# Kernel tuning notes

Hardware: AMD Instinct MI355X
Metric: run time of the kernel (lower is better)

Reference implementation:

```python
import jax, jax.numpy as jnp
import numpy as np
from jax import lax


def setup_inputs() -> dict:
    key = jax.random.key(0)
    k1, k2 = jax.random.split(key)
    N, dim, m = 8192, 1024, 1024
    x = jax.random.normal(k1, (N, dim), dtype=jnp.float32)
    vectors = jax.random.normal(k2, (m, dim), dtype=jnp.float32) * 0.01
    bias = jnp.zeros((dim,), dtype=jnp.float32)
    return {"x": x, "vectors": vectors, "bias": bias}


def reference(x, vectors, bias):
    # Normalize each reflection vector to unit length: [m, d]
    v_normed = vectors / jnp.linalg.norm(vectors, axis=1, keepdims=True)

    def step(out, v):
        # out: [N, d], v: [d]
        proj = out @ v                       # [N]
        out = out - 2.0 * proj[:, None] * v  # rank-1 Householder update
        return out, None

    out, _ = lax.scan(step, x, v_normed)
    return out + bias
```

## Files before the change

### kernel.cpp

```cpp
#include <hip/hip_runtime.h>
#include <hip/hip_bf16.h>

typedef __attribute__((ext_vector_type(8))) short short8;
typedef __attribute__((ext_vector_type(4))) short s16x4;
typedef __attribute__((ext_vector_type(4))) float f32x4;

static __device__ inline short f2bf(float f) {
    unsigned u = __float_as_uint(f);
    unsigned r = (u + 0x7fffu + ((u >> 16) & 1u)) >> 16;
    return (short)r;
}
static __device__ inline float bf2f(short h) {
    return __uint_as_float(((unsigned)(unsigned short)h) << 16);
}

static __device__ inline int swz32(int row, int slot) {
    return row * 32 + ((slot ^ ((row >> 1) & 3)) << 3);
}
static __device__ inline int swz64(int row, int slot) {
    return row * 64 + ((slot ^ (row & 7)) << 3);
}

__global__ __launch_bounds__(256) void k_prepall(const float* __restrict__ vec,
                                                 short* __restrict__ Vh,
                                                 short* __restrict__ Vth,
                                                 int m, int dim) {
    __shared__ float tile[8][1028];
    __shared__ float ps[8][32];
    __shared__ float invs[8];
    int r0 = blockIdx.x * 8;
    int t = threadIdx.x;
    int rt = t >> 5, ct = t & 31;
    float ss = 0.f;
#pragma unroll
    for (int p = 0; p < 8; ++p) {
        int c = p * 128 + ct * 4;
        float4 v = *(const float4*)&vec[(size_t)(r0 + rt) * dim + c];
        *(float4*)&tile[rt][c] = v;
        ss += v.x * v.x + v.y * v.y + v.z * v.z + v.w * v.w;
    }
    ps[rt][ct] = ss;
    __syncthreads();
    if (t < 8) {
        float s = 0.f;
#pragma unroll
        for (int q = 0; q < 32; ++q) s += ps[t][q];
        invs[t] = 1.0f / sqrtf(s);
    }
    __syncthreads();
    float iv = invs[rt];
#pragma unroll
    for (int p = 0; p < 8; ++p) {
        int c = p * 128 + ct * 4;
        s16x4 h;
#pragma unroll
        for (int q = 0; q < 4; ++q) h[q] = f2bf(tile[rt][c + q] * iv);
        *(s16x4*)&Vh[(size_t)(r0 + rt) * dim + c] = h;
    }
#pragma unroll
    for (int cc = 0; cc < 4; ++cc) {
        int c = t * 4 + cc;
        s16x4 h0, h1;
#pragma unroll
        for (int r = 0; r < 4; ++r) h0[r] = f2bf(tile[r][c] * invs[r]);
#pragma unroll
        for (int r = 0; r < 4; ++r) h1[r] = f2bf(tile[4 + r][c] * invs[4 + r]);
        *(s16x4*)&Vth[(size_t)c * m + r0] = h0;
        *(s16x4*)&Vth[(size_t)c * m + r0 + 4] = h1;
    }
}

template<int MODE, int TRI, int CH>
__global__ __launch_bounds__(256) void k_nt64pc(
    const short* __restrict__ Ah, const short* __restrict__ Al,
    const short* __restrict__ Bh, const short* __restrict__ Bl,
    float* __restrict__ Cf, short* __restrict__ Ch, short* __restrict__ Cl,
    int K, int lda, int ldb, int ldc, int gw, int nTiles,
    const float* __restrict__ castX, short* __restrict__ castXh, int castN4) {
    __shared__ short As[2][2][64 * 32];
    __shared__ short Bs[2][2][64 * 32];
    int flat = blockIdx.x;
    if (flat >= nTiles) {
        int idx = (flat - nTiles) * 256 + threadIdx.x;
        int stride = (gridDim.x - nTiles) * 256;
        for (int i = idx; i < castN4; i += stride) {
            float4 v = ((const float4*)castX)[i];
            float f[4] = {v.x, v.y, v.z, v.w};
            s16x4 h;
#pragma unroll
            for (int q = 0; q < 4; ++q) h[q] = f2bf(f[q]);
            *(s16x4*)&castXh[(size_t)i * 4] = h;
        }
        return;
    }
    int i0 = (flat / gw) * 64, j0 = (flat % gw) * 64;
    if (TRI == 2 && j0 < i0) return;
    int KE = (TRI == 1) ? (j0 + 64) : K;
    int t = threadIdx.x, lane = t & 63, wave = t >> 6;
    int wr = wave >> 1, wc = wave & 1;
    int srow = t >> 2, slot = t & 3;
    int sofs = swz32(srow, slot);
    int gofs = slot * 8;
    const short* gA_h = &Ah[(size_t)(i0 + srow) * lda + gofs];
    const short* gA_l = (CH >= 3) ? &Al[(size_t)(i0 + srow) * lda + gofs] : nullptr;
    const short* gB_h = &Bh[(size_t)(j0 + srow) * ldb + gofs];
    const short* gB_l = (CH >= 2) ? &Bl[(size_t)(j0 + srow) * ldb + gofs] : nullptr;
    short8 pAh = *(const short8*)&gA_h[0];
    short8 pAl, pBl;
    short8 pBh = *(const short8*)&gB_h[0];
    if (CH >= 2) pBl = *(const short8*)&gB_l[0];
    if (CH >= 3) pAl = *(const short8*)&gA_l[0];
    *(short8*)&As[0][0][sofs] = pAh;
    *(short8*)&Bs[0][0][sofs] = pBh;
    if (CH >= 2) *(short8*)&Bs[0][1][sofs] = pBl;
    if (CH >= 3) *(short8*)&As[0][1][sofs] = pAl;
    f32x4 acc[2][2] = {};
    int nIter = KE >> 5;
    int cur = 0;
    for (int it = 0; it < nIter; ++it) {
        __syncthreads();
        int kn = (it + 1) << 5;
        bool have = kn < KE;
        if (have) {
            pAh = *(const short8*)&gA_h[kn];
            pBh = *(const short8*)&gB_h[kn];
            if (CH >= 2) pBl = *(const short8*)&gB_l[kn];
            if (CH >= 3) pAl = *(const short8*)&gA_l[kn];
        }
        int g = lane >> 4;
        short8 ah[2], al2[2], bh[2], bl2[2];
#pragma unroll
        for (int i = 0; i < 2; ++i) {
            int ro = swz32(wr * 32 + i * 16 + (lane & 15), g);
            ah[i] = *(const short8*)&As[cur][0][ro];
            if (CH >= 3) al2[i] = *(const short8*)&As[cur][1][ro];
        }
#pragma unroll
        for (int j = 0; j < 2; ++j) {
            int ro = swz32(wc * 32 + j * 16 + (lane & 15), g);
            bh[j] = *(const short8*)&Bs[cur][0][ro];
            if (CH >= 2) bl2[j] = *(const short8*)&Bs[cur][1][ro];
        }
#pragma unroll
        for (int i = 0; i < 2; ++i)
#pragma unroll
            for (int j = 0; j < 2; ++j) {
                acc[i][j] = __builtin_amdgcn_mfma_f32_16x16x32_bf16(ah[i], bh[j], acc[i][j], 0, 0, 0);
                if (CH >= 2)
                    acc[i][j] = __builtin_amdgcn_mfma_f32_16x16x32_bf16(ah[i], bl2[j], acc[i][j], 0, 0, 0);
                if (CH >= 3)
                    acc[i][j] = __builtin_amdgcn_mfma_f32_16x16x32_bf16(al2[i], bh[j], acc[i][j], 0, 0, 0);
            }
        if (have) {
            *(short8*)&As[cur ^ 1][0][sofs] = pAh;
            *(short8*)&Bs[cur ^ 1][0][sofs] = pBh;
            if (CH >= 2) *(short8*)&Bs[cur ^ 1][1][sofs] = pBl;
            if (CH >= 3) *(short8*)&As[cur ^ 1][1][sofs] = pAl;
        }
        cur ^= 1;
    }
#pragma unroll
    for (int i = 0; i < 2; ++i)
#pragma unroll
        for (int j = 0; j < 2; ++j) {
            int row0 = i0 + wr * 32 + i * 16 + ((lane >> 4) << 2);
            int col = j0 + wc * 32 + j * 16 + (lane & 15);
#pragma unroll
            for (int r = 0; r < 4; ++r) {
                float v = acc[i][j][r];
                size_t idx = (size_t)(row0 + r) * ldc + col;
                if (MODE == 2) {
                    Ch[idx] = f2bf((((row0 + r) == col) ? 1.f : 0.f) - v);
                } else if (MODE == 1) {
                    Ch[idx] = f2bf(v);
                } else {
                    short h = f2bf(v);
                    Ch[idx] = h;
                    Cl[idx] = f2bf(v - bf2f(h));
                    Cf[idx] = v;
                }
            }
        }
}

__global__ __launch_bounds__(256) void k_baseinv2(const float* __restrict__ G,
                                                  short* __restrict__ Th, short* __restrict__ Tl,
                                                  short* __restrict__ Tth, short* __restrict__ Ttl,
                                                  int m) {
    __shared__ float Rs[64 * 64];
    int d = blockIdx.x >> 4, g = blockIdx.x & 15;
    int b0 = d * 64;
    int t = threadIdx.x, lane = t & 63, wave = t >> 6;
    {
        int r = t >> 2, c00 = (t & 3) * 16;
#pragma unroll
        for (int q = 0; q < 4; ++q)
            *(float4*)&Rs[r * 64 + c00 + q * 4] =
                *(const float4*)&G[(size_t)(b0 + r) * m + b0 + c00 + q * 4];
    }
    __syncthreads();
    int c = g * 4 + wave;
    float x = 0.f;
    for (int r = c; r >= 0; --r) {
        float prod = Rs[r * 64 + lane] * x;
        float s = prod;
#pragma unroll
        for (int off = 32; off; off >>= 1) s += __shfl_xor(s, off, 64);
        if (lane == r) x = ((r == c) ? 2.f : 0.f) - 2.f * s;
    }
    short h = f2bf(x);
    short l = f2bf(x - bf2f(h));
    Th[(size_t)(b0 + lane) * m + b0 + c] = h;
    Tl[(size_t)(b0 + lane) * m + b0 + c] = l;
    Tth[(size_t)(b0 + c) * m + b0 + lane] = h;
    Ttl[(size_t)(b0 + c) * m + b0 + lane] = l;
}

__global__ __launch_bounds__(256) void k_tree64f(const float* __restrict__ G,
                                                 short* __restrict__ Th, short* __restrict__ Tl,
                                                 short* __restrict__ Tth, short* __restrict__ Ttl,
                                                 int m) {
    __shared__ float Gb[64 * 65];
    __shared__ float Ai[64 * 65];
    __shared__ float Ci[64 * 64];
    __shared__ float Tm[64 * 64];
    int p = blockIdx.x;
    int a0 = p * 128, c0 = a0 + 64;
    int t = threadIdx.x;
    {
        int r = t >> 2, c00 = (t & 3) * 16;
#pragma unroll
        for (int q = 0; q < 4; ++q) {
            *(float4*)&Gb[r * 65 + c00 + q * 4] =
                *(const float4*)&G[(size_t)(a0 + r) * m + c0 + c00 + q * 4];
            s16x4 ha = *(const s16x4*)&Th[(size_t)(a0 + r) * m + a0 + c00 + q * 4];
            s16x4 la = *(const s16x4*)&Tl[(size_t)(a0 + r) * m + a0 + c00 + q * 4];
            s16x4 hc = *(const s16x4*)&Th[(size_t)(c0 + r) * m + c0 + c00 + q * 4];
            s16x4 lc = *(const s16x4*)&Tl[(size_t)(c0 + r) * m + c0 + c00 + q * 4];
#pragma unroll
            for (int e = 0; e < 4; ++e) {
                Ai[r * 65 + c00 + q * 4 + e] = bf2f(ha[e]) + bf2f(la[e]);
                Ci[r * 64 + c00 + q * 4 + e] = bf2f(hc[e]) + bf2f(lc[e]);
            }
        }
    }
    __syncthreads();
    int tx = t & 15, ty = t >> 4;
    float acc[4][4] = {};
#pragma unroll 4
    for (int k = 0; k < 64; ++k) {
        float av[4], bv[4];
#pragma unroll
        for (int i = 0; i < 4; ++i) av[i] = Gb[(ty * 4 + i) * 65 + k];
#pragma unroll
        for (int j = 0; j < 4; ++j) bv[j] = Ci[k * 64 + tx * 4 + j];
#pragma unroll
        for (int i = 0; i < 4; ++i)
#pragma unroll
            for (int j = 0; j < 4; ++j) acc[i][j] += av[i] * bv[j];
    }
#pragma unroll
    for (int i = 0; i < 4; ++i)
#pragma unroll
        for (int j = 0; j < 4; ++j) Tm[(ty * 4 + i) * 64 + tx * 4 + j] = acc[i][j];
    __syncthreads();
    float acc2[4][4] = {};
#pragma unroll 4
    for (int k = 0; k < 64; ++k) {
        float av[4], bv[4];
#pragma unroll
        for (int i = 0; i < 4; ++i) av[i] = Ai[(ty * 4 + i) * 65 + k];
#pragma unroll
        for (int j = 0; j < 4; ++j) bv[j] = Tm[k * 64 + tx * 4 + j];
#pragma unroll
        for (int i = 0; i < 4; ++i)
#pragma unroll
            for (int j = 0; j < 4; ++j) acc2[i][j] += av[i] * bv[j];
    }
#pragma unroll
    for (int i = 0; i < 4; ++i)
#pragma unroll
        for (int j = 0; j < 4; ++j) {
            float v = -acc2[i][j];
            short h = f2bf(v);
            short l = f2bf(v - bf2f(h));
            int R = a0 + ty * 4 + i, C = c0 + tx * 4 + j;
            Th[(size_t)R * m + C] = h;
            Tl[(size_t)R * m + C] = l;
            Tth[(size_t)C * m + R] = h;
            Ttl[(size_t)C * m + R] = l;
        }
}

template<int PHASE>
__global__ __launch_bounds__(256) void k_trimm(
    const short* __restrict__ Ah, const short* __restrict__ Al,
    const short* __restrict__ Bh, const short* __restrict__ Bl,
    short* __restrict__ C1h, short* __restrict__ C1l,
    short* __restrict__ C2h, short* __restrict__ C2l,
    int m, int s) {
    __shared__ short As[2][64 * 32];
    __shared__ short Bs[2][64 * 32];
    int p = blockIdx.z;
    int a0 = 2 * p * s, c0 = a0 + s;
    int r0 = blockIdx.y * 64, ct = blockIdx.x * 64;
    int KS = (PHASE == 1) ? 0 : r0;
    int KE = (PHASE == 1) ? (ct + 64) : s;
    size_t tbase = (size_t)p * s * s;
    int t = threadIdx.x, lane = t & 63, wave = t >> 6;
    int wr = wave >> 1, wc = wave & 1;
    int srow = t >> 2, slot = t & 3;
    int sofs = swz32(srow, slot);
    int gofs = slot * 8;
    f32x4 acc[2][2] = {};
    for (int k0 = KS; k0 < KE; k0 += 32) {
        __syncthreads();
        if (PHASE == 1) {
            *(short8*)&As[0][sofs] = *(const short8*)&Ah[(size_t)(a0 + r0 + srow) * m + c0 + k0 + gofs];
            *(short8*)&As[1][sofs] = *(const short8*)&Al[(size_t)(a0 + r0 + srow) * m + c0 + k0 + gofs];
            *(short8*)&Bs[0][sofs] = *(const short8*)&Bh[(size_t)(c0 + ct + srow) * m + c0 + k0 + gofs];
            *(short8*)&Bs[1][sofs] = *(const short8*)&Bl[(size_t)(c0 + ct + srow) * m + c0 + k0 + gofs];
        } else {
            *(short8*)&As[0][sofs] = *(const short8*)&Ah[(size_t)(a0 + r0 + srow) * m + a0 + k0 + gofs];
            *(short8*)&As[1][sofs] = *(const short8*)&Al[(size_t)(a0 + r0 + srow) * m + a0 + k0 + gofs];
            *(short8*)&Bs[0][sofs] = *(const short8*)&Bh[tbase + (size_t)(ct + srow) * s + k0 + gofs];
            *(short8*)&Bs[1][sofs] = *(const short8*)&Bl[tbase + (size_t)(ct + srow) * s + k0 + gofs];
        }
        __syncthreads();
        int g = lane >> 4;
        short8 ah[2], al2[2], bh[2], bl2[2];
#pragma unroll
        for (int i = 0; i < 2; ++i) {
            int ro = swz32(wr * 32 + i * 16 + (lane & 15), g);
            ah[i] = *(const short8*)&As[0][ro];
            al2[i] = *(const short8*)&As[1][ro];
        }
#pragma unroll
        for (int j = 0; j < 2; ++j) {
            int ro = swz32(wc * 32 + j * 16 + (lane & 15), g);
            bh[j] = *(const short8*)&Bs[0][ro];
            bl2[j] = *(const short8*)&Bs[1][ro];
        }
#pragma unroll
        for (int i = 0; i < 2; ++i)
#pragma unroll
            for (int j = 0; j < 2; ++j) {
                acc[i][j] = __builtin_amdgcn_mfma_f32_16x16x32_bf16(ah[i], bh[j], acc[i][j], 0, 0, 0);
                acc[i][j] = __builtin_amdgcn_mfma_f32_16x16x32_bf16(ah[i], bl2[j], acc[i][j], 0, 0, 0);
                acc[i][j] = __builtin_amdgcn_mfma_f32_16x16x32_bf16(al2[i], bh[j], acc[i][j], 0, 0, 0);
            }
    }
#pragma unroll
    for (int i = 0; i < 2; ++i)
#pragma unroll
        for (int j = 0; j < 2; ++j) {
            int row0 = r0 + wr * 32 + i * 16 + ((lane >> 4) << 2);
            int col = ct + wc * 32 + j * 16 + (lane & 15);
#pragma unroll
            for (int r = 0; r < 4; ++r) {
                if (PHASE == 1) {
                    float v = acc[i][j][r];
                    short h = f2bf(v);
                    short l = f2bf(v - bf2f(h));
                    size_t idx = tbase + (size_t)col * s + row0 + r;
                    C1h[idx] = h;
                    C1l[idx] = l;
                } else {
                    float v = -acc[i][j][r];
                    short h = f2bf(v);
                    short l = f2bf(v - bf2f(h));
                    int R = a0 + row0 + r, Cc = c0 + col;
                    C1h[(size_t)R * m + Cc] = h;
                    C1l[(size_t)R * m + Cc] = l;
                    C2h[(size_t)Cc * m + R] = h;
                    C2l[(size_t)Cc * m + R] = l;
                }
            }
        }
}

__global__ __launch_bounds__(256) void k_apply3(const short* __restrict__ xh,
                                                const short* __restrict__ Qt,
                                                const float* __restrict__ bias,
                                                float* __restrict__ out, int dim) {
    __shared__ short As[128 * 64];
    __shared__ short Bs[128 * 64];
    int nwg = gridDim.x * gridDim.y;
    int flat = blockIdx.y * gridDim.x + blockIdx.x;
    int cpx = nwg >> 3;
    int L = (flat & 7) * cpx + (flat >> 3);
    int m0 = (L / gridDim.x) * 128, n0 = (L % gridDim.x) * 128;
    int t = threadIdx.x, lane = t & 63, wave = t >> 6;
    int wr = wave >> 1, wc = wave & 1;
    int sr = lane >> 3;
    int sslot = (lane & 7) ^ (sr & 7);
    f32x4 acc[4][4] = {};
    for (int k0 = 0; k0 < dim; k0 += 64) {
        __syncthreads();
#pragma unroll
        for (int q = 0; q < 4; ++q) {
            int rg = wave * 4 + q;
            int row = rg * 8 + sr;
            const short* gA = &xh[(size_t)(m0 + row) * dim + k0 + sslot * 8];
            const short* gB = &Qt[(size_t)(n0 + row) * dim + k0 + sslot * 8];
            __builtin_amdgcn_global_load_lds(
                (const __attribute__((address_space(1))) void*)gA,
                (__attribute__((address_space(3))) void*)&As[rg * 8 * 64], 16, 0, 0);
            __builtin_amdgcn_global_load_lds(
                (const __attribute__((address_space(1))) void*)gB,
                (__attribute__((address_space(3))) void*)&Bs[rg * 8 * 64], 16, 0, 0);
        }
        __syncthreads();
#pragma unroll
        for (int kk = 0; kk < 2; ++kk) {
            int g = kk * 4 + (lane >> 4);
            short8 af[4], bf_[4];
#pragma unroll
            for (int i = 0; i < 4; ++i)
                af[i] = *(const short8*)&As[swz64(wr * 64 + i * 16 + (lane & 15), g)];
#pragma unroll
            for (int j = 0; j < 4; ++j)
                bf_[j] = *(const short8*)&Bs[swz64(wc * 64 + j * 16 + (lane & 15), g)];
#pragma unroll
            for (int i = 0; i < 4; ++i)
#pragma unroll
                for (int j = 0; j < 4; ++j)
                    acc[i][j] = __builtin_amdgcn_mfma_f32_16x16x32_bf16(af[i], bf_[j], acc[i][j], 0, 0, 0);
        }
    }
#pragma unroll
    for (int i = 0; i < 4; ++i)
#pragma unroll
        for (int j = 0; j < 4; ++j) {
            int row = m0 + wr * 64 + i * 16 + (lane >> 4) * 4;
            int col = n0 + wc * 64 + j * 16 + (lane & 15);
            float b = bias[col];
#pragma unroll
            for (int r = 0; r < 4; ++r)
                out[(size_t)(row + r) * dim + col] = acc[i][j][r] + b;
        }
}

extern "C" void kernel_launch(void* const* d_in, const int* in_sizes, int n_in,
                              void* d_out, int out_size, void* d_ws, size_t ws_size,
                              hipStream_t stream) {
    const float* x = (const float*)d_in[0];
    const float* vec = (const float*)d_in[1];
    const float* bias = (const float*)d_in[2];
    float* out = (float*)d_out;

    int dim = in_sizes[2];
    int m = in_sizes[1] / dim;
    int n = in_sizes[0] / dim;

    const size_t MD = (size_t)m * dim;
    const size_t MM = (size_t)m * m;

    char* cur = (char*)d_ws;
    auto alloc_f = [&](size_t nelem) { float* p = (float*)cur; cur += nelem * 4; return p; };
    auto alloc_s = [&](size_t nelem) { short* p = (short*)cur; cur += nelem * 2; return p; };
    float* G   = alloc_f(MM);
    short* Vh  = alloc_s(MD);
    short* Vth = alloc_s(MD);
    short* Gh  = alloc_s(MM);
    short* Gl  = alloc_s(MM);
    short* Th  = alloc_s(MM);
    short* Tl  = alloc_s(MM);
    short* Tth = alloc_s(MM);
    short* Ttl = alloc_s(MM);
    short* Wh  = alloc_s(MD);
    short* Qt  = alloc_s((size_t)dim * dim);
    short* tmph = alloc_s(MM / 2);
    short* tmpl = alloc_s(MM / 2);
    short* xh  = alloc_s((size_t)n * dim);

    int gw = m / 64;
    int nTiles = gw * gw;
    int castN4 = (int)((size_t)n * dim / 4);

    k_prepall<<<m / 8, 256, 0, stream>>>(vec, Vh, Vth, m, dim);

    k_nt64pc<3, 2, 1><<<nTiles + 512, 256, 0, stream>>>(Vh, nullptr, Vh, nullptr, G, Gh, Gl,
                                                        dim, dim, dim, m, gw, nTiles,
                                                        x, xh, castN4);
    k_baseinv2<<<(m / 64) * 16, 256, 0, stream>>>(G, Th, Tl, Tth, Ttl, m);
    k_tree64f<<<m / 128, 256, 0, stream>>>(G, Th, Tl, Tth, Ttl, m);
    for (int s = 128; s < m; s <<= 1) {
        dim3 g(s / 64, s / 64, m / (2 * s));
        k_trimm<1><<<g, 256, 0, stream>>>(Gh, Gl, Tth, Ttl, tmph, tmpl, nullptr, nullptr, m, s);
        k_trimm<2><<<g, 256, 0, stream>>>(Th, Tl, tmph, tmpl, Th, Tl, Tth, Ttl, m, s);
    }

    k_nt64pc<1, 1, 2><<<(m / 64) * (dim / 64), 256, 0, stream>>>(Vth, nullptr, Tth, Ttl, nullptr, Wh, nullptr,
                                                                 m, m, m, m, m / 64, (m / 64) * (dim / 64),
                                                                 nullptr, nullptr, 0);
    k_nt64pc<2, 0, 1><<<(dim / 64) * (dim / 64), 256, 0, stream>>>(Vth, nullptr, Wh, nullptr, nullptr, Qt, nullptr,
                                                                   m, m, m, dim, dim / 64, (dim / 64) * (dim / 64),
                                                                   nullptr, nullptr, 0);

    k_apply3<<<dim3(dim / 128, n / 128), 256, 0, stream>>>(xh, Qt, bias, out, dim);
}
```

Baseline: 150.1 us.

## Fuse triangular-inverse tree stages into one persistent kernel with grid barriers

Replaces the base-inverse kernel, the 64-block tree kernel and the sequence of per-level trimm launches with a single persistent kernel. Its 256 blocks synchronize through an atomic-counter global barrier, and the counter is zeroed inside the preceding Gram kernel. This removes about 16 kernel launch gaps on a chain of small, latency-bound stages. In exchange it depends on all 256 blocks being co-resident, and the spin barrier has a timeout guard that could silently break correctness if residency fails.

```diff
diff --git a/kernel.cpp b/kernel.cpp
--- a/kernel.cpp
+++ b/kernel.cpp
@@ -19,6 +19,21 @@
 }
 static __device__ inline int swz64(int row, int slot) {
     return row * 64 + ((slot ^ (row & 7)) << 3);
+}
+
+static __device__ inline void gbar(unsigned* cnt, unsigned target) {
+    __syncthreads();
+    if (threadIdx.x == 0) {
+        __threadfence();
+        __hip_atomic_fetch_add(cnt, 1u, __ATOMIC_ACQ_REL, __HIP_MEMORY_SCOPE_AGENT);
+        long guard = 0;
+        while (__hip_atomic_load(cnt, __ATOMIC_ACQUIRE, __HIP_MEMORY_SCOPE_AGENT) < target) {
+            __builtin_amdgcn_s_sleep(2);
+            if (++guard > (1L << 25)) break;
+        }
+        __threadfence();
+    }
+    __syncthreads();
 }
 
 __global__ __launch_bounds__(256) void k_prepall(const float* __restrict__ vec,
@@ -76,11 +91,13 @@
     const short* __restrict__ Bh, const short* __restrict__ Bl,
     float* __restrict__ Cf, short* __restrict__ Ch, short* __restrict__ Cl,
     int K, int lda, int ldb, int ldc, int gw, int nTiles,
-    const float* __restrict__ castX, short* __restrict__ castXh, int castN4) {
+    const float* __restrict__ castX, short* __restrict__ castXh, int castN4,
+    unsigned* zeroCnt) {
     __shared__ short As[2][2][64 * 32];
     __shared__ short Bs[2][2][64 * 32];
     int flat = blockIdx.x;
     if (flat >= nTiles) {
+        if (zeroCnt && flat == nTiles && threadIdx.x == 0) *zeroCnt = 0u;
         int idx = (flat - nTiles) * 256 + threadIdx.x;
         int stride = (gridDim.x - nTiles) * 256;
         for (int i = idx; i < castN4; i += stride) {
@@ -183,127 +200,16 @@
         }
 }
 
-__global__ __launch_bounds__(256) void k_baseinv2(const float* __restrict__ G,
-                                                  short* __restrict__ Th, short* __restrict__ Tl,
-                                                  short* __restrict__ Tth, short* __restrict__ Ttl,
-                                                  int m) {
-    __shared__ float Rs[64 * 64];
-    int d = blockIdx.x >> 4, g = blockIdx.x & 15;
-    int b0 = d * 64;
-    int t = threadIdx.x, lane = t & 63, wave = t >> 6;
-    {
-        int r = t >> 2, c00 = (t & 3) * 16;
-#pragma unroll
-        for (int q = 0; q < 4; ++q)
-            *(float4*)&Rs[r * 64 + c00 + q * 4] =
-                *(const float4*)&G[(size_t)(b0 + r) * m + b0 + c00 + q * 4];
-    }
-    __syncthreads();
-    int c = g * 4 + wave;
-    float x = 0.f;
-    for (int r = c; r >= 0; --r) {
-        float prod = Rs[r * 64 + lane] * x;
-        float s = prod;
-#pragma unroll
-        for (int off = 32; off; off >>= 1) s += __shfl_xor(s, off, 64);
-        if (lane == r) x = ((r == c) ? 2.f : 0.f) - 2.f * s;
-    }
-    short h = f2bf(x);
-    short l = f2bf(x - bf2f(h));
-    Th[(size_t)(b0 + lane) * m + b0 + c] = h;
-    Tl[(size_t)(b0 + lane) * m + b0 + c] = l;
-    Tth[(size_t)(b0 + c) * m + b0 + lane] = h;
-    Ttl[(size_t)(b0 + c) * m + b0 + lane] = l;
-}
-
-__global__ __launch_bounds__(256) void k_tree64f(const float* __restrict__ G,
-                                                 short* __restrict__ Th, short* __restrict__ Tl,
-                                                 short* __restrict__ Tth, short* __restrict__ Ttl,
-                                                 int m) {
-    __shared__ float Gb[64 * 65];
-    __shared__ float Ai[64 * 65];
-    __shared__ float Ci[64 * 64];
-    __shared__ float Tm[64 * 64];
-    int p = blockIdx.x;
-    int a0 = p * 128, c0 = a0 + 64;
-    int t = threadIdx.x;
-    {
-        int r = t >> 2, c00 = (t & 3) * 16;
-#pragma unroll
-        for (int q = 0; q < 4; ++q) {
-            *(float4*)&Gb[r * 65 + c00 + q * 4] =
-                *(const float4*)&G[(size_t)(a0 + r) * m + c0 + c00 + q * 4];
-            s16x4 ha = *(const s16x4*)&Th[(size_t)(a0 + r) * m + a0 + c00 + q * 4];
-            s16x4 la = *(const s16x4*)&Tl[(size_t)(a0 + r) * m + a0 + c00 + q * 4];
-            s16x4 hc = *(const s16x4*)&Th[(size_t)(c0 + r) * m + c0 + c00 + q * 4];
-            s16x4 lc = *(const s16x4*)&Tl[(size_t)(c0 + r) * m + c0 + c00 + q * 4];
-#pragma unroll
-            for (int e = 0; e < 4; ++e) {
-                Ai[r * 65 + c00 + q * 4 + e] = bf2f(ha[e]) + bf2f(la[e]);
-                Ci[r * 64 + c00 + q * 4 + e] = bf2f(hc[e]) + bf2f(lc[e]);
-            }
-        }
-    }
-    __syncthreads();
-    int tx = t & 15, ty = t >> 4;
-    float acc[4][4] = {};
-#pragma unroll 4
-    for (int k = 0; k < 64; ++k) {
-        float av[4], bv[4];
-#pragma unroll
-        for (int i = 0; i < 4; ++i) av[i] = Gb[(ty * 4 + i) * 65 + k];
-#pragma unroll
-        for (int j = 0; j < 4; ++j) bv[j] = Ci[k * 64 + tx * 4 + j];
-#pragma unroll
-        for (int i = 0; i < 4; ++i)
-#pragma unroll
-            for (int j = 0; j < 4; ++j) acc[i][j] += av[i] * bv[j];
-    }
-#pragma unroll
-    for (int i = 0; i < 4; ++i)
-#pragma unroll
-        for (int j = 0; j < 4; ++j) Tm[(ty * 4 + i) * 64 + tx * 4 + j] = acc[i][j];
-    __syncthreads();
-    float acc2[4][4] = {};
-#pragma unroll 4
-    for (int k = 0; k < 64; ++k) {
-        float av[4], bv[4];
-#pragma unroll
-        for (int i = 0; i < 4; ++i) av[i] = Ai[(ty * 4 + i) * 65 + k];
-#pragma unroll
-        for (int j = 0; j < 4; ++j) bv[j] = Tm[k * 64 + tx * 4 + j];
-#pragma unroll
-        for (int i = 0; i < 4; ++i)
-#pragma unroll
-            for (int j = 0; j < 4; ++j) acc2[i][j] += av[i] * bv[j];
-    }
-#pragma unroll
-    for (int i = 0; i < 4; ++i)
-#pragma unroll
-        for (int j = 0; j < 4; ++j) {
-            float v = -acc2[i][j];
-            short h = f2bf(v);
-            short l = f2bf(v - bf2f(h));
-            int R = a0 + ty * 4 + i, C = c0 + tx * 4 + j;
-            Th[(size_t)R * m + C] = h;
-            Tl[(size_t)R * m + C] = l;
-            Tth[(size_t)C * m + R] = h;
-            Ttl[(size_t)C * m + R] = l;
-        }
-}
-
 template<int PHASE>
-__global__ __launch_bounds__(256) void k_trimm(
+static __device__ void trimm_tile(
+    short* As0, short* As1, short* Bs0, short* Bs1,
     const short* __restrict__ Ah, const short* __restrict__ Al,
     const short* __restrict__ Bh, const short* __restrict__ Bl,
     short* __restrict__ C1h, short* __restrict__ C1l,
     short* __restrict__ C2h, short* __restrict__ C2l,
-    int m, int s) {
-    __shared__ short As[2][64 * 32];
-    __shared__ short Bs[2][64 * 32];
-    int p = blockIdx.z;
+    int m, int s, int p, int r0t, int ctt) {
     int a0 = 2 * p * s, c0 = a0 + s;
-    int r0 = blockIdx.y * 64, ct = blockIdx.x * 64;
+    int r0 = r0t * 64, ct = ctt * 64;
     int KS = (PHASE == 1) ? 0 : r0;
     int KE = (PHASE == 1) ? (ct + 64) : s;
     size_t tbase = (size_t)p * s * s;
@@ -316,15 +222,15 @@
     for (int k0 = KS; k0 < KE; k0 += 32) {
         __syncthreads();
         if (PHASE == 1) {
-            *(short8*)&As[0][sofs] = *(const short8*)&Ah[(size_t)(a0 + r0 + srow) * m + c0 + k0 + gofs];
-            *(short8*)&As[1][sofs] = *(const short8*)&Al[(size_t)(a0 + r0 + srow) * m + c0 + k0 + gofs];
-            *(short8*)&Bs[0][sofs] = *(const short8*)&Bh[(size_t)(c0 + ct + srow) * m + c0 + k0 + gofs];
-            *(short8*)&Bs[1][sofs] = *(const short8*)&Bl[(size_t)(c0 + ct + srow) * m + c0 + k0 + gofs];
+            *(short8*)&As0[sofs] = *(const short8*)&Ah[(size_t)(a0 + r0 + srow) * m + c0 + k0 + gofs];
+            *(short8*)&As1[sofs] = *(const short8*)&Al[(size_t)(a0 + r0 + srow) * m + c0 + k0 + gofs];
+            *(short8*)&Bs0[sofs] = *(const short8*)&Bh[(size_t)(c0 + ct + srow) * m + c0 + k0 + gofs];
+            *(short8*)&Bs1[sofs] = *(const short8*)&Bl[(size_t)(c0 + ct + srow) * m + c0 + k0 + gofs];
         } else {
-            *(short8*)&As[0][sofs] = *(const short8*)&Ah[(size_t)(a0 + r0 + srow) * m + a0 + k0 + gofs];
-            *(short8*)&As[1][sofs] = *(const short8*)&Al[(size_t)(a0 + r0 + srow) * m + a0 + k0 + gofs];
-            *(short8*)&Bs[0][sofs] = *(const short8*)&Bh[tbase + (size_t)(ct + srow) * s + k0 + gofs];
-            *(short8*)&Bs[1][sofs] = *(const short8*)&Bl[tbase + (size_t)(ct + srow) * s + k0 + gofs];
+            *(short8*)&As0[sofs] = *(const short8*)&Ah[(size_t)(a0 + r0 + srow) * m + a0 + k0 + gofs];
+            *(short8*)&As1[sofs] = *(const short8*)&Al[(size_t)(a0 + r0 + srow) * m + a0 + k0 + gofs];
+            *(short8*)&Bs0[sofs] = *(const short8*)&Bh[tbase + (size_t)(ct + srow) * s + k0 + gofs];
+            *(short8*)&Bs1[sofs] = *(const short8*)&Bl[tbase + (size_t)(ct + srow) * s + k0 + gofs];
         }
         __syncthreads();
         int g = lane >> 4;
@@ -332,14 +238,14 @@
 #pragma unroll
         for (int i = 0; i < 2; ++i) {
             int ro = swz32(wr * 32 + i * 16 + (lane & 15), g);
-            ah[i] = *(const short8*)&As[0][ro];
-            al2[i] = *(const short8*)&As[1][ro];
+            ah[i] = *(const short8*)&As0[ro];
+            al2[i] = *(const short8*)&As1[ro];
         }
 #pragma unroll
         for (int j = 0; j < 2; ++j) {
             int ro = swz32(wc * 32 + j * 16 + (lane & 15), g);
-            bh[j] = *(const short8*)&Bs[0][ro];
-            bl2[j] = *(const short8*)&Bs[1][ro];
+            bh[j] = *(const short8*)&Bs0[ro];
+            bl2[j] = *(const short8*)&Bs1[ro];
         }
 #pragma unroll
         for (int i = 0; i < 2; ++i)
@@ -379,6 +285,142 @@
         }
 }
 
+__global__ __launch_bounds__(256) void k_tree_all(
+    const float* __restrict__ G, const short* __restrict__ Gh, const short* __restrict__ Gl,
+    short* __restrict__ Th, short* __restrict__ Tl,
+    short* __restrict__ Tth, short* __restrict__ Ttl,
+    short* __restrict__ tmph, short* __restrict__ tmpl,
+    unsigned* cnt, int m) {
+    __shared__ __align__(16) char ldsraw[66048];
+    int bid = blockIdx.x;
+    unsigned NB = gridDim.x;
+    int t = threadIdx.x, lane = t & 63, wave = t >> 6;
+
+    {
+        float* Rs = (float*)ldsraw;
+        int d = bid >> 4, g = bid & 15;
+        int b0 = d * 64;
+        {
+            int r = t >> 2, c00 = (t & 3) * 16;
+#pragma unroll
+            for (int q = 0; q < 4; ++q)
+                *(float4*)&Rs[r * 64 + c00 + q * 4] =
+                    *(const float4*)&G[(size_t)(b0 + r) * m + b0 + c00 + q * 4];
+        }
+        __syncthreads();
+        int c = g * 4 + wave;
+        float x = 0.f;
+        for (int r = c; r >= 0; --r) {
+            float s = Rs[r * 64 + lane] * x;
+#pragma unroll
+            for (int off = 32; off; off >>= 1) s += __shfl_xor(s, off, 64);
+            if (lane == r) x = ((r == c) ? 2.f : 0.f) - 2.f * s;
+        }
+        short h = f2bf(x);
+        short l = f2bf(x - bf2f(h));
+        Th[(size_t)(b0 + lane) * m + b0 + c] = h;
+        Tl[(size_t)(b0 + lane) * m + b0 + c] = l;
+        Tth[(size_t)(b0 + c) * m + b0 + lane] = h;
+        Ttl[(size_t)(b0 + c) * m + b0 + lane] = l;
+    }
+    gbar(cnt, NB * 1);
+
+    if (bid < m / 128) {
+        float* Gb = (float*)ldsraw;
+        float* Ai = Gb + 64 * 65;
+        float* Ci = Ai + 64 * 65;
+        float* Tm = Ci + 64 * 64;
+        int p = bid;
+        int a0 = p * 128, c0 = a0 + 64;
+        {
+            int r = t >> 2, c00 = (t & 3) * 16;
+#pragma unroll
+            for (int q = 0; q < 4; ++q) {
+                *(float4*)&Gb[r * 65 + c00 + q * 4] =
+                    *(const float4*)&G[(size_t)(a0 + r) * m + c0 + c00 + q * 4];
+                s16x4 ha = *(const s16x4*)&Th[(size_t)(a0 + r) * m + a0 + c00 + q * 4];
+                s16x4 la = *(const s16x4*)&Tl[(size_t)(a0 + r) * m + a0 + c00 + q * 4];
+                s16x4 hc = *(const s16x4*)&Th[(size_t)(c0 + r) * m + c0 + c00 + q * 4];
+                s16x4 lc = *(const s16x4*)&Tl[(size_t)(c0 + r) * m + c0 + c00 + q * 4];
+#pragma unroll
+                for (int e = 0; e < 4; ++e) {
+                    Ai[r * 65 + c00 + q * 4 + e] = bf2f(ha[e]) + bf2f(la[e]);
+                    Ci[r * 64 + c00 + q * 4 + e] = bf2f(hc[e]) + bf2f(lc[e]);
+                }
+            }
+        }
+        __syncthreads();
+        int tx = t & 15, ty = t >> 4;
+        float acc[4][4] = {};
+#pragma unroll 4
+        for (int k = 0; k < 64; ++k) {
+            float av[4], bv[4];
+#pragma unroll
+            for (int i = 0; i < 4; ++i) av[i] = Gb[(ty * 4 + i) * 65 + k];
+#pragma unroll
+            for (int j = 0; j < 4; ++j) bv[j] = Ci[k * 64 + tx * 4 + j];
+#pragma unroll
+            for (int i = 0; i < 4; ++i)
+#pragma unroll
+                for (int j = 0; j < 4; ++j) acc[i][j] += av[i] * bv[j];
+        }
+#pragma unroll
+        for (int i = 0; i < 4; ++i)
+#pragma unroll
+            for (int j = 0; j < 4; ++j) Tm[(ty * 4 + i) * 64 + tx * 4 + j] = acc[i][j];
+        __syncthreads();
+        float acc2[4][4] = {};
+#pragma unroll 4
+        for (int k = 0; k < 64; ++k) {
+            float av[4], bv[4];
+#pragma unroll
+            for (int i = 0; i < 4; ++i) av[i] = Ai[(ty * 4 + i) * 65 + k];
+#pragma unroll
+            for (int j = 0; j < 4; ++j) bv[j] = Tm[k * 64 + tx * 4 + j];
+#pragma unroll
+            for (int i = 0; i < 4; ++i)
+#pragma unroll
+                for (int j = 0; j < 4; ++j) acc2[i][j] += av[i] * bv[j];
+        }
+#pragma unroll
+        for (int i = 0; i < 4; ++i)
+#pragma unroll
+            for (int j = 0; j < 4; ++j) {
+                float v = -acc2[i][j];
+                short h = f2bf(v);
+                short l = f2bf(v - bf2f(h));
+                int R = a0 + ty * 4 + i, C = c0 + tx * 4 + j;
+                Th[(size_t)R * m + C] = h;
+                Tl[(size_t)R * m + C] = l;
+                Tth[(size_t)C * m + R] = h;
+                Ttl[(size_t)C * m + R] = l;
+            }
+    }
+    gbar(cnt, NB * 2);
+
+    short* As0 = (short*)ldsraw;
+    short* As1 = As0 + 2048;
+    short* Bs0 = As1 + 2048;
+    short* Bs1 = Bs0 + 2048;
+    unsigned phase = 2;
+    for (int s = 128; s < m; s <<= 1) {
+        int tilesX = s / 64;
+        int ntiles = tilesX * tilesX * (m / (2 * s));
+        if (bid < ntiles) {
+            int ctt = bid % tilesX, r0t = (bid / tilesX) % tilesX, p = bid / (tilesX * tilesX);
+            trimm_tile<1>(As0, As1, Bs0, Bs1, Gh, Gl, Tth, Ttl,
+                          tmph, tmpl, nullptr, nullptr, m, s, p, r0t, ctt);
+        }
+        gbar(cnt, NB * (++phase));
+        if (bid < ntiles) {
+            int ctt = bid % tilesX, r0t = (bid / tilesX) % tilesX, p = bid / (tilesX * tilesX);
+            trimm_tile<2>(As0, As1, Bs0, Bs1, Th, Tl, tmph, tmpl,
+                          Th, Tl, Tth, Ttl, m, s, p, r0t, ctt);
+        }
+        gbar(cnt, NB * (++phase));
+    }
+}
+
 __global__ __launch_bounds__(256) void k_apply3(const short* __restrict__ xh,
                                                 const short* __restrict__ Qt,
                                                 const float* __restrict__ bias,
@@ -460,6 +502,7 @@
     auto alloc_f = [&](size_t nelem) { float* p = (float*)cur; cur += nelem * 4; return p; };
     auto alloc_s = [&](size_t nelem) { short* p = (short*)cur; cur += nelem * 2; return p; };
     float* G   = alloc_f(MM);
+    unsigned* cnt = (unsigned*)alloc_f(4);
     short* Vh  = alloc_s(MD);
     short* Vth = alloc_s(MD);
     short* Gh  = alloc_s(MM);
@@ -482,21 +525,16 @@
 
     k_nt64pc<3, 2, 1><<<nTiles + 512, 256, 0, stream>>>(Vh, nullptr, Vh, nullptr, G, Gh, Gl,
                                                         dim, dim, dim, m, gw, nTiles,
-                                                        x, xh, castN4);
-    k_baseinv2<<<(m / 64) * 16, 256, 0, stream>>>(G, Th, Tl, Tth, Ttl, m);
-    k_tree64f<<<m / 128, 256, 0, stream>>>(G, Th, Tl, Tth, Ttl, m);
-    for (int s = 128; s < m; s <<= 1) {
-        dim3 g(s / 64, s / 64, m / (2 * s));
-        k_trimm<1><<<g, 256, 0, stream>>>(Gh, Gl, Tth, Ttl, tmph, tmpl, nullptr, nullptr, m, s);
-        k_trimm<2><<<g, 256, 0, stream>>>(Th, Tl, tmph, tmpl, Th, Tl, Tth, Ttl, m, s);
-    }
+                                                        x, xh, castN4, cnt);
+    k_tree_all<<<(m / 64) * 16, 256, 0, stream>>>(G, Gh, Gl, Th, Tl, Tth, Ttl,
+                                                  tmph, tmpl, cnt, m);
 
     k_nt64pc<1, 1, 2><<<(m / 64) * (dim / 64), 256, 0, stream>>>(Vth, nullptr, Tth, Ttl, nullptr, Wh, nullptr,
                                                                  m, m, m, m, m / 64, (m / 64) * (dim / 64),
-                                                                 nullptr, nullptr, 0);
+                                                                 nullptr, nullptr, 0, nullptr);
     k_nt64pc<2, 0, 1><<<(dim / 64) * (dim / 64), 256, 0, stream>>>(Vth, nullptr, Wh, nullptr, nullptr, Qt, nullptr,
                                                                    m, m, m, dim, dim / 64, (dim / 64) * (dim / 64),
-                                                                   nullptr, nullptr, 0);
+                                                                   nullptr, nullptr, 0, nullptr);
 
     k_apply3<<<dim3(dim / 128, n / 128), 256, 0, stream>>>(xh, Qt, bias, out, dim);
 }
```

Measured after the change: 535.1 us. 257% more time.
